# Performance work log

Hardware: AMD Instinct MI355X
Metric: run time of the kernel (lower is better)

Reference implementation:

```python
import jax, jax.numpy as jnp
import numpy as np

ALPHA = 0.2  # LeakyReLU negative slope
NEG_INF = -9e15  # matches torch's -9000000000000000.0 mask value


def setup_inputs() -> dict:
    key = jax.random.key(0)
    k1, k2, k3, k4 = jax.random.split(key, 4)
    B, M, F = 8, 1024, 256
    H, E = 8, F // 8  # attention_heads, out_features
    x = jax.random.normal(k1, (B, M, F), dtype=jnp.float32)
    adj = jax.random.randint(k2, (B, M, M), 0, 2, dtype=jnp.int32)
    weight = jax.random.normal(k3, (H, F, E), dtype=jnp.float32)
    att = jax.random.normal(k4, (H, 2 * E, 1), dtype=jnp.float32)
    return {"x": x, "adj": adj, "weight": weight, "att": att}


def reference(x, adj, weight, att):
    # x: [B, M, F], adj: [B, M, M], weight: [H, F, E], att: [H, 2E, 1]
    B, M, _ = x.shape
    H, _, E = weight.shape
    Wh = jnp.einsum('bmf,hfe->bhme', x, weight)  # [B, H, M, E]
    # Decompose the repeat+concat score: e_ij = a1.Wh_i + a2.Wh_j
    a1 = att[:, :E, 0]   # [H, E]
    a2 = att[:, E:, 0]   # [H, E]
    s1 = jnp.einsum('bhme,he->bhm', Wh, a1)
    s2 = jnp.einsum('bhme,he->bhm', Wh, a2)
    e = s1[:, :, :, None] + s2[:, :, None, :]  # [B, H, M, M]
    e = jnp.where(e > 0, e, ALPHA * e)  # LeakyReLU
    e = jnp.where(adj[:, None, :, :] > 0, e, NEG_INF)
    attn = jax.nn.softmax(e, axis=-1)  # [B, H, M, M]
    h = jnp.einsum('bhmn,bhne->bhme', attn, Wh)  # [B, H, M, E]
    out = h.transpose(0, 2, 1, 3).reshape(B, M, H * E)  # concat heads
    out = jax.nn.elu(out)  # res_pre_act path (dropout is identity in eval)
    return out
```

## Files before the change

### kernel.cpp

```cpp
#include <hip/hip_runtime.h>
#include <stdint.h>

#define ALPHA 0.2f
#define LOG2E 1.44269504089f
#define SKIP_THR 24.0f

typedef __attribute__((ext_vector_type(8))) short s16x8;
typedef __attribute__((ext_vector_type(4))) float f32x4;
typedef __attribute__((ext_vector_type(4))) unsigned u32x4;

__device__ __forceinline__ unsigned short f2bf(float f) {
    union { float f; unsigned u; } c; c.f = f;
    unsigned u = c.u;
    u += 0x7fffu + ((u >> 16) & 1u);
    return (unsigned short)(u >> 16);
}

__global__ void k_prep_w(const float* __restrict__ weight, const float* __restrict__ att,
                         unsigned short* __restrict__ wT, float* __restrict__ wa1,
                         float* __restrict__ wa2) {
    int blk = blockIdx.x, t = threadIdx.x;
    if (blk < 256) {
        int c = blk, h = c >> 5, e = c & 31;
        wT[c * 256 + t] = f2bf(weight[h * 8192 + t * 32 + e]);
    } else {
        int id = blk - 256, h = id >> 1, which = id & 1;
        float s = 0.f;
        for (int e = 0; e < 32; ++e)
            s += weight[h * 8192 + t * 32 + e] * att[h * 64 + which * 32 + e];
        s *= LOG2E;
        (which ? wa2 : wa1)[h * 256 + t] = s;
    }
}

__global__ void __launch_bounds__(512) k_pre(const int* __restrict__ adj,
                                             unsigned* __restrict__ gmask,
                                             const float* __restrict__ x,
                                             const unsigned short* __restrict__ wT,
                                             const float* __restrict__ wa1,
                                             const float* __restrict__ wa2,
                                             float* __restrict__ s1,
                                             float* __restrict__ s2,
                                             unsigned short* __restrict__ WhT) {
    __shared__ unsigned char adjb[16][1024];
    __shared__ float xs[16][260];
    __shared__ unsigned short x16s[16][256];
    int blk = blockIdx.x;
    int t = threadIdx.x, w = t >> 6, l = t & 63;
    int b = blk >> 6;
    const int* abase = adj + blk * 16384;
#pragma unroll
    for (int it = 0; it < 8; ++it) {
        int f = it * 512 + t;
        int4 v = *(const int4*)(abase + f * 4);
        int row = f >> 8, col = (f & 255) * 4;
        unsigned p1 = __builtin_amdgcn_perm((unsigned)v.y, (unsigned)v.x, 0x00000400u);
        unsigned p2 = __builtin_amdgcn_perm((unsigned)v.w, (unsigned)v.z, 0x00000400u);
        unsigned pk = __builtin_amdgcn_perm(p2, p1, 0x05040100u);
        *(unsigned*)&adjb[row][col ^ ((row & 7) << 4)] = pk;
    }
    const float* xbase = x + blk * 4096;
#pragma unroll
    for (int it = 0; it < 2; ++it) {
        int f = it * 512 + t;
        float4 xv = *(const float4*)(xbase + f * 4);
        int row = f >> 6, col = (f & 63) * 4;
        *(float4*)&xs[row][col] = xv;
        ushort4 hv;
        hv.x = f2bf(xv.x); hv.y = f2bf(xv.y); hv.z = f2bf(xv.z); hv.w = f2bf(xv.w);
        *(ushort4*)((char*)&x16s[0][0] + ((row * 512 + col * 2) ^ ((row & 7) << 4))) = hv;
    }
    __syncthreads();
    if (w < 4) {
        for (int k = 0; k < 64; ++k) {
            int task = w * 64 + k;
            int row = task >> 4, ch = task & 15;
            unsigned char byv = adjb[row][(ch * 64 + l) ^ ((row & 7) << 4)];
            unsigned long long mk = __ballot(byv != 0);
            if (l == 0) {
                unsigned* dst = gmask + (blk * 16 + row) * 32 + ch * 2;
                dst[0] = (unsigned)mk;
                dst[1] = (unsigned)(mk >> 32);
            }
        }
    } else {
        int td = (w - 4) * 64 + l;
        int row = td & 15, grp = td >> 4;
        int h = grp >> 1, which = grp & 1;
        const float* wap = (which ? wa2 : wa1) + h * 256;
        float s = 0.f;
#pragma unroll 4
        for (int f = 0; f < 256; f += 4) {
            f32x4 xv = *(const f32x4*)&xs[row][f];
            f32x4 wv = *(const f32x4*)&wap[f];
            s += xv[0] * wv[0] + xv[1] * wv[1] + xv[2] * wv[2] + xv[3] * wv[3];
        }
        int m = (blk & 63) * 16 + row;
        (which ? s2 : s1)[(b * 8 + h) * 1024 + m] = s;
    }
    int lrow = l & 15, lk = l >> 4;
#pragma unroll
    for (int ct = 0; ct < 2; ++ct) {
        int c0 = (w * 2 + ct) * 16;
        f32x4 acc = {0, 0, 0, 0};
        const unsigned short* ap = wT + (c0 + lrow) * 256 + lk * 8;
#pragma unroll
        for (int k0 = 0; k0 < 256; k0 += 32) {
            s16x8 af = *(const s16x8*)(ap + k0);
            s16x8 bf = *(const s16x8*)((char*)&x16s[0][0] +
                        ((lrow * 512 + (lk * 8 + k0) * 2) ^ ((lrow & 7) << 4)));
            acc = __builtin_amdgcn_mfma_f32_16x16x32_bf16(af, bf, acc, 0, 0, 0);
        }
#pragma unroll
        for (int j = 0; j < 4; ++j) {
            int c = c0 + lk * 4 + j;
            WhT[(b * 256 + c) * 1024 + (blk & 63) * 16 + lrow] = f2bf(acc[j]);
        }
    }
}

__global__ void __launch_bounds__(64) k_top(const float* __restrict__ s2,
                                            float* __restrict__ tval,
                                            unsigned* __restrict__ tidx) {
    int bh = blockIdx.x, l = threadIdx.x;
    const float* p = s2 + bh * 1024;
    float v[16];
#pragma unroll
    for (int k = 0; k < 4; ++k) {
        f32x4 x4 = *(const f32x4*)(p + l * 16 + k * 4);
        v[k * 4 + 0] = x4[0]; v[k * 4 + 1] = x4[1];
        v[k * 4 + 2] = x4[2]; v[k * 4 + 3] = x4[3];
    }
    unsigned used = 0;
    for (int r = 0; r < 16; ++r) {
        float lmax = -3.0e38f; int larg = 0;
#pragma unroll
        for (int k = 0; k < 16; ++k) {
            float c = ((used >> k) & 1u) ? -3.0e38f : v[k];
            if (c > lmax) { lmax = c; larg = k; }
        }
        float wmax = lmax;
#pragma unroll
        for (int off = 32; off >= 1; off >>= 1) wmax = fmaxf(wmax, __shfl_xor(wmax, off));
        unsigned long long hm = __ballot(lmax == wmax);
        int fl = (int)__builtin_ctzll(hm);
        if (l == fl) {
            tval[bh * 16 + r] = wmax;
            tidx[bh * 16 + r] = (unsigned)(l * 16 + larg);
            used |= 1u << larg;
        }
    }
}

__global__ void __launch_bounds__(256, 4) k_attn(const unsigned* __restrict__ gmask,
                                                 const float* __restrict__ s1,
                                                 const float* __restrict__ s2,
                                                 const float* __restrict__ tval,
                                                 const unsigned* __restrict__ tidx,
                                                 const unsigned short* __restrict__ WhT,
                                                 float* __restrict__ out) {
    __shared__ unsigned amaskw[16][36];
    __shared__ float s1s[4][16];
    __shared__ float ptmx[4][32][4];
    __shared__ float tmx[4][32];
    int bid = blockIdx.x;
    int o = (bid & 7) * 128 + (bid >> 3);
    int b = o >> 7, r = o & 127;
    int mt = r >> 1, m0 = mt * 16, hg = (r & 1) * 4;
    int t = threadIdx.x, w = t >> 6, l = t & 63;
    for (int i = t; i < 512; i += 256)
        amaskw[i >> 5][i & 31] = gmask[(b * 1024 + m0) * 32 + i];
    if (t < 64) s1s[t >> 4][t & 15] = s1[b * 8192 + (hg + (t >> 4)) * 1024 + m0 + (t & 15)];
#pragma unroll
    for (int it = 0; it < 2; ++it) {
        int task = it * 256 + t;
        int hd2 = task >> 7, rem = task & 127, tile = rem >> 2, part = rem & 3;
        const float* sp = s2 + b * 8192 + (hg + hd2) * 1024 + tile * 32 + part * 8;
        f32x4 a = *(const f32x4*)sp;
        f32x4 c = *(const f32x4*)(sp + 4);
        ptmx[hd2][tile][part] = fmaxf(fmaxf(fmaxf(a[0], a[1]), fmaxf(a[2], a[3])),
                                      fmaxf(fmaxf(c[0], c[1]), fmaxf(c[2], c[3])));
    }
    __syncthreads();
    if (t < 128) {
        int hd2 = t >> 5, tile = t & 31;
        tmx[hd2][tile] = fmaxf(fmaxf(ptmx[hd2][tile][0], ptmx[hd2][tile][1]),
                               fmaxf(ptmx[hd2][tile][2], ptmx[hd2][tile][3]));
    }
    __syncthreads();
    int m = l & 15, q = l >> 4;
    int h = hg + w;
    f32x4 tm[8];
#pragma unroll
    for (int k = 0; k < 8; ++k) tm[k] = *(const f32x4*)&tmx[w][k * 4];
    const float*    tv = tval + (b * 8 + h) * 16;
    const unsigned* ti = tidx + (b * 8 + h) * 16;
    float mxs2 = tv[15];
#pragma unroll
    for (int j = 0; j < 16; ++j) {
        unsigned id = ti[j];
        unsigned wd = amaskw[m][id >> 5];
        unsigned bit = (wd >> (id & 31u)) & 1u;
        mxs2 = fmaxf(mxs2, bit ? tv[j] : -3.0e38f);
    }
    float s1v = s1s[w][m];
    float mxr = s1v + mxs2;
    float mx = fmaxf(mxr, ALPHA * mxr);
    float cc1 = s1v - mx;
    float cc2 = fmaf(ALPHA, s1v, -mx);
    f32x4 acc0 = {0,0,0,0}, acc1 = {0,0,0,0}, accs = {0,0,0,0};
    s16x8 ones;
#pragma unroll
    for (int u = 0; u < 8; ++u) ones[u] = (short)0x3F80;
    const float* sgb = s2 + (b * 8 + h) * 1024 + q * 8;
    const unsigned short* bp0 = WhT + (b * 8 + h) * 32768 + m * 1024 + q * 8;
    const unsigned short* bp1 = bp0 + 16 * 1024;
#pragma unroll
    for (int i = 0; i < 32; ++i) {
        float tmf = tm[i >> 2][i & 3];
        float ub = fmaxf(tmf + cc1, fmaf(ALPHA, tmf, cc2));
        if (__any(ub >= -SKIP_THR)) {
            int n0 = i * 32;
            unsigned wm8 = amaskw[m][i] >> (q * 8);
            f32x4 svA = *(const f32x4*)(sgb + n0);
            f32x4 svB = *(const f32x4*)(sgb + n0 + 4);
            float pv[8];
#pragma unroll
            for (int u = 0; u < 8; ++u) {
                float sv = (u < 4 ? svA[u] : svB[u - 4]);
                float arg = fmaxf(sv + cc1, fmaf(ALPHA, sv, cc2));
                arg = ((wm8 >> u) & 1u) ? arg : -3.0e38f;
                pv[u] = __builtin_amdgcn_exp2f(arg);
            }
            u32x4 aw;
#pragma unroll
            for (int p = 0; p < 4; ++p) {
                union { float f; unsigned u; } lo, hi;
                lo.f = pv[2 * p]; hi.f = pv[2 * p + 1];
                aw[p] = __builtin_amdgcn_perm(hi.u, lo.u, 0x07060302u);
            }
            s16x8 af = __builtin_bit_cast(s16x8, aw);
            s16x8 bf0 = *(const s16x8*)(bp0 + n0);
            s16x8 bf1 = *(const s16x8*)(bp1 + n0);
            acc0 = __builtin_amdgcn_mfma_f32_16x16x32_bf16(af, bf0, acc0, 0, 0, 0);
            acc1 = __builtin_amdgcn_mfma_f32_16x16x32_bf16(af, bf1, acc1, 0, 0, 0);
            accs = __builtin_amdgcn_mfma_f32_16x16x32_bf16(af, ones, accs, 0, 0, 0);
        }
    }
#pragma unroll
    for (int j = 0; j < 4; ++j) {
        float inv = 1.f / accs[j];
        float v0 = acc0[j] * inv;
        float v1 = acc1[j] * inv;
        v0 = v0 > 0.f ? v0 : __expf(v0) - 1.f;
        v1 = v1 > 0.f ? v1 : __expf(v1) - 1.f;
        int mrow = q * 4 + j;
        float* op = &out[(b * 1024 + m0 + mrow) * 256 + h * 32];
        op[m] = v0;
        op[16 + m] = v1;
    }
}

extern "C" void kernel_launch(void* const* d_in, const int* in_sizes, int n_in,
                              void* d_out, int out_size, void* d_ws, size_t ws_size,
                              hipStream_t stream) {
    const float* x      = (const float*)d_in[0];
    const int*   adj    = (const int*)d_in[1];
    const float* weight = (const float*)d_in[2];
    const float* att    = (const float*)d_in[3];

    char* ws = (char*)d_ws;
    unsigned short* wT  = (unsigned short*)(ws);
    unsigned short* WhT = (unsigned short*)(ws + 131072);
    float* s1  = (float*)(ws + 4325376);
    float* s2  = (float*)(ws + 4587520);
    float* wa1 = (float*)(ws + 4849664);
    float* wa2 = (float*)(ws + 4857856);
    unsigned* gmask = (unsigned*)(ws + 4866048);
    float*    tval  = (float*)(ws + 5914624);
    unsigned* tidx  = (unsigned*)(ws + 5918720);
    float* out = (float*)d_out;

    k_prep_w<<<272, 256, 0, stream>>>(weight, att, wT, wa1, wa2);
    k_pre<<<512, 512, 0, stream>>>(adj, gmask, x, wT, wa1, wa2, s1, s2, WhT);
    k_top<<<64, 64, 0, stream>>>(s2, tval, tidx);
    k_attn<<<1024, 256, 0, stream>>>(gmask, s1, s2, tval, tidx, WhT, out);
}
```

Before: 63.30 us.

## Process all eight heads per attention block and split dot-product accumulators

k_attn now launches 512 blocks of 512 threads, each covering all 8 heads for a 16-row tile instead of 4 heads. The adjacency mask tile and the s2 tile-max preprocessing are therefore loaded and computed once per row tile rather than twice. The top-k value and index loads become vectorized, and the s1/s2 dot product in k_pre uses four independent accumulators to shorten the dependency chain. Larger blocks may cut occupancy or register budget under the new launch bounds and halve the number of blocks available for scheduling.

```diff
diff --git a/kernel.cpp b/kernel.cpp
--- a/kernel.cpp
+++ b/kernel.cpp
@@ -88,13 +88,23 @@
         int row = td & 15, grp = td >> 4;
         int h = grp >> 1, which = grp & 1;
         const float* wap = (which ? wa2 : wa1) + h * 256;
-        float s = 0.f;
-#pragma unroll 4
-        for (int f = 0; f < 256; f += 4) {
-            f32x4 xv = *(const f32x4*)&xs[row][f];
-            f32x4 wv = *(const f32x4*)&wap[f];
-            s += xv[0] * wv[0] + xv[1] * wv[1] + xv[2] * wv[2] + xv[3] * wv[3];
-        }
+        float sa0 = 0.f, sa1 = 0.f, sa2 = 0.f, sa3 = 0.f;
+#pragma unroll
+        for (int f = 0; f < 256; f += 16) {
+            f32x4 x0 = *(const f32x4*)&xs[row][f];
+            f32x4 w0 = *(const f32x4*)&wap[f];
+            f32x4 x1 = *(const f32x4*)&xs[row][f + 4];
+            f32x4 w1 = *(const f32x4*)&wap[f + 4];
+            f32x4 x2 = *(const f32x4*)&xs[row][f + 8];
+            f32x4 w2 = *(const f32x4*)&wap[f + 8];
+            f32x4 x3 = *(const f32x4*)&xs[row][f + 12];
+            f32x4 w3 = *(const f32x4*)&wap[f + 12];
+            sa0 += x0[0]*w0[0] + x0[1]*w0[1] + x0[2]*w0[2] + x0[3]*w0[3];
+            sa1 += x1[0]*w1[0] + x1[1]*w1[1] + x1[2]*w1[2] + x1[3]*w1[3];
+            sa2 += x2[0]*w2[0] + x2[1]*w2[1] + x2[2]*w2[2] + x2[3]*w2[3];
+            sa3 += x3[0]*w3[0] + x3[1]*w3[1] + x3[2]*w3[2] + x3[3]*w3[3];
+        }
+        float s = (sa0 + sa1) + (sa2 + sa3);
         int m = (blk & 63) * 16 + row;
         (which ? s2 : s1)[(b * 8 + h) * 1024 + m] = s;
     }
@@ -152,7 +162,7 @@
     }
 }
 
-__global__ void __launch_bounds__(256, 4) k_attn(const unsigned* __restrict__ gmask,
+__global__ void __launch_bounds__(512, 4) k_attn(const unsigned* __restrict__ gmask,
                                                  const float* __restrict__ s1,
                                                  const float* __restrict__ s2,
                                                  const float* __restrict__ tval,
@@ -160,48 +170,52 @@
                                                  const unsigned short* __restrict__ WhT,
                                                  float* __restrict__ out) {
     __shared__ unsigned amaskw[16][36];
-    __shared__ float s1s[4][16];
-    __shared__ float ptmx[4][32][4];
-    __shared__ float tmx[4][32];
+    __shared__ float s1s[8][16];
+    __shared__ float ptmx[8][32][4];
+    __shared__ float tmx[8][32];
     int bid = blockIdx.x;
-    int o = (bid & 7) * 128 + (bid >> 3);
-    int b = o >> 7, r = o & 127;
-    int mt = r >> 1, m0 = mt * 16, hg = (r & 1) * 4;
+    int o = (bid & 7) * 64 + (bid >> 3);
+    int b = o >> 6, mt = o & 63, m0 = mt * 16;
     int t = threadIdx.x, w = t >> 6, l = t & 63;
-    for (int i = t; i < 512; i += 256)
-        amaskw[i >> 5][i & 31] = gmask[(b * 1024 + m0) * 32 + i];
-    if (t < 64) s1s[t >> 4][t & 15] = s1[b * 8192 + (hg + (t >> 4)) * 1024 + m0 + (t & 15)];
+    amaskw[t >> 5][t & 31] = gmask[(b * 1024 + m0) * 32 + t];
+    if (t < 128) s1s[t >> 4][t & 15] = s1[b * 8192 + (t >> 4) * 1024 + m0 + (t & 15)];
 #pragma unroll
     for (int it = 0; it < 2; ++it) {
-        int task = it * 256 + t;
+        int task = it * 512 + t;
         int hd2 = task >> 7, rem = task & 127, tile = rem >> 2, part = rem & 3;
-        const float* sp = s2 + b * 8192 + (hg + hd2) * 1024 + tile * 32 + part * 8;
+        const float* sp = s2 + b * 8192 + hd2 * 1024 + tile * 32 + part * 8;
         f32x4 a = *(const f32x4*)sp;
         f32x4 c = *(const f32x4*)(sp + 4);
         ptmx[hd2][tile][part] = fmaxf(fmaxf(fmaxf(a[0], a[1]), fmaxf(a[2], a[3])),
                                       fmaxf(fmaxf(c[0], c[1]), fmaxf(c[2], c[3])));
     }
     __syncthreads();
-    if (t < 128) {
+    if (t < 256) {
         int hd2 = t >> 5, tile = t & 31;
         tmx[hd2][tile] = fmaxf(fmaxf(ptmx[hd2][tile][0], ptmx[hd2][tile][1]),
                                fmaxf(ptmx[hd2][tile][2], ptmx[hd2][tile][3]));
     }
     __syncthreads();
     int m = l & 15, q = l >> 4;
-    int h = hg + w;
+    int h = w;
     f32x4 tm[8];
 #pragma unroll
     for (int k = 0; k < 8; ++k) tm[k] = *(const f32x4*)&tmx[w][k * 4];
     const float*    tv = tval + (b * 8 + h) * 16;
     const unsigned* ti = tidx + (b * 8 + h) * 16;
-    float mxs2 = tv[15];
+    f32x4 tvv[4]; u32x4 tiv[4];
+#pragma unroll
+    for (int k = 0; k < 4; ++k) {
+        tvv[k] = *(const f32x4*)(tv + k * 4);
+        tiv[k] = *(const u32x4*)(ti + k * 4);
+    }
+    float mxs2 = tvv[3][3];
 #pragma unroll
     for (int j = 0; j < 16; ++j) {
-        unsigned id = ti[j];
+        unsigned id = tiv[j >> 2][j & 3];
         unsigned wd = amaskw[m][id >> 5];
         unsigned bit = (wd >> (id & 31u)) & 1u;
-        mxs2 = fmaxf(mxs2, bit ? tv[j] : -3.0e38f);
+        mxs2 = fmaxf(mxs2, bit ? tvv[j >> 2][j & 3] : -3.0e38f);
     }
     float s1v = s1s[w][m];
     float mxr = s1v + mxs2;
@@ -284,5 +298,5 @@
     k_prep_w<<<272, 256, 0, stream>>>(weight, att, wT, wa1, wa2);
     k_pre<<<512, 512, 0, stream>>>(adj, gmask, x, wT, wa1, wa2, s1, s2, WhT);
     k_top<<<64, 64, 0, stream>>>(s2, tval, tidx);
-    k_attn<<<1024, 256, 0, stream>>>(gmask, s1, s2, tval, tidx, WhT, out);
-}
+    k_attn<<<512, 512, 0, stream>>>(gmask, s1, s2, tval, tidx, WhT, out);
+}
```

New measurement: 63.54 us. No clear change (+0.4%).
